# Optimization experiments

Measured on AMD Instinct MI355X. Metric: run time of the kernel, lower is better.

The kernel has to match this reference:

```python
import jax, jax.numpy as jnp
import numpy as np

B, S, D = 16, 1024, 1024
LR = 0.01  # manual SGD step size inside TTT


def setup_inputs() -> dict:
    key = jax.random.key(0)
    ks = jax.random.split(key, 9)
    s = 1.0 / np.sqrt(D)  # nn.Linear default init range
    lin = lambda k: jax.random.uniform(k, (D, D), jnp.float32, -s, s)
    return {
        "x": jax.random.normal(ks[0], (B, S, D), jnp.float32),
        "noise": jax.random.normal(ks[1], (B, S, D), jnp.float32),
        "alpha1": jax.random.normal(ks[2], (D,), jnp.float32),
        "alpha2": jax.random.normal(ks[3], (D,), jnp.float32),
        "W_map": lin(ks[4]),    # TTT.mapping weight (updated online)
        "W_state": lin(ks[5]),  # TTT.State weight
        "W_probe": lin(ks[6]),  # TTT.Probe weight
        "W_p1": lin(ks[7]),     # GatingUnit.proj_1
        "W_p2": lin(ks[8]),     # GatingUnit.proj_2
    }


def reference(x, noise, alpha1, alpha2, W_map, W_state, W_probe, W_p1, W_p2):
    # --- TTT: sequential per-timestep test-time training, expressed as a scan ---
    def ttt(h):
        xs = jnp.swapaxes(h, 0, 1)       # [S, B, D]
        ns = jnp.swapaxes(noise, 0, 1)   # [S, B, D]

        def step(W, inp):
            x_t, n_t = inp                       # [B, D]
            state = x_t @ W_state.T              # State(x_t)
            tv = state + n_t                     # train_view = state + randn
            err = tv @ W.T - state               # mapping(train_view) - label_view
            # d(mse)/dW for y = x W^T, loss = mean(err^2) over B*D elements
            grad = (2.0 / (x_t.shape[0] * x_t.shape[1])) * (err.T @ tv)
            Wn = W - LR * grad                   # manual SGD update
            readout = (x_t @ W_probe.T) @ Wn.T   # mapping(Probe(x_t)) with updated W
            return Wn, readout

        _, outs = jax.lax.scan(step, W_map, (xs, ns))
        return jnp.swapaxes(outs, 0, 1)          # [B, S, D]

    # --- TensorMapperBlock ---
    res = x
    h = jnp.tanh(alpha1 * x)          # VecDyT norm_1
    x1 = ttt(h) + res
    res2 = x1
    h2 = jnp.tanh(alpha2 * x1)        # VecDyT norm_2
    u = jax.nn.gelu(h2 @ W_p1.T, approximate=False)  # torch nn.GELU (exact)
    v = h2 @ W_p2.T
    return u * v + res2
```

## Files before the change

kernel.cpp:

```cpp
#include <hip/hip_runtime.h>
#include <math.h>


typedef __bf16 bf16;
typedef __attribute__((ext_vector_type(8))) __bf16 bf16x8;
typedef __attribute__((ext_vector_type(4))) __bf16 bf16x4;
typedef __attribute__((ext_vector_type(4))) float f32x4;

#define LAM 1.220703125e-6f

enum { M_TV = 0, M_P = 1, M_E0 = 2, M_CT = 3, M_KP = 4, M_OUT = 5, M_U = 6 };

struct GA {
  const bf16* A;  int lda;
  const bf16* B;  int ldb;
  const bf16* A2; int lda2;
  const bf16* B2; int ldb2;
  int K;
  const float* noise;
  const float* xin;
  const float* alpha2;
  const bf16* TVb;
  const bf16* Vb;
  bf16* H2b;
  float* outf;
  bf16* Cb; int ldc;
};

#define GLOAD_LDS16(gp, lp)                                                   \
  __builtin_amdgcn_global_load_lds(                                           \
      (const __attribute__((address_space(1))) unsigned int*)(gp),            \
      (__attribute__((address_space(3))) unsigned int*)(lp), 16, 0, 0)

__device__ __forceinline__ void stage_tiles(const bf16* __restrict__ Ap, int lda,
                                            const bf16* __restrict__ Bp, int ldb,
                                            int k0, bf16* As, bf16* Bs, int tid) {
  const int wv = tid >> 6, lane = tid & 63;
#pragma unroll
  for (int i = 0; i < 2; ++i) {
    int idx = (wv << 6) + lane + (i << 8);
    int row = idx >> 2;
    int k8 = (idx & 3) << 3;
    int lbase = ((wv << 6) + (i << 8)) << 3;
    GLOAD_LDS16(Ap + (size_t)row * lda + k0 + k8, As + lbase);
    GLOAD_LDS16(Bp + (size_t)row * ldb + k0 + k8, Bs + lbase);
  }
}

__device__ __forceinline__ void compute_step(const bf16* As, const bf16* Bs,
                                             int wr, int wc, int m, int ko,
                                             f32x4 acc[4][4]) {
  bf16x8 af[4], bfr[4];
#pragma unroll
  for (int i = 0; i < 4; ++i)
    af[i] = *(const bf16x8*)(As + (wr + i * 16 + m) * 32 + ko * 8);
#pragma unroll
  for (int j = 0; j < 4; ++j)
    bfr[j] = *(const bf16x8*)(Bs + (wc + j * 16 + m) * 32 + ko * 8);
#pragma unroll
  for (int i = 0; i < 4; ++i) {
#pragma unroll
    for (int j = 0; j < 4; ++j)
      acc[i][j] =
          __builtin_amdgcn_mfma_f32_16x16x32_bf16(af[i], bfr[j], acc[i][j], 0, 0, 0);
  }
}

template <int MODE>
__device__ __forceinline__ void stage_sel(const GA& g, int s, int steps1,
                                          const bf16* A1, const bf16* B1,
                                          const bf16* A2, const bf16* B2,
                                          bf16* Asb, bf16* Bsb, int tid) {
  if constexpr (MODE == M_OUT) {
    if (s >= steps1) {
      stage_tiles(A2, g.lda2, B2, g.ldb2, (s - steps1) << 5, Asb, Bsb, tid);
      return;
    }
  }
  stage_tiles(A1, g.lda, B1, g.ldb, s << 5, Asb, Bsb, tid);
}

template <int MODE>
__global__ __launch_bounds__(256) void gemm_nt(GA g) {
  __shared__ __attribute__((aligned(16))) bf16 As0[128 * 32];
  __shared__ __attribute__((aligned(16))) bf16 Bs0[128 * 32];
  __shared__ __attribute__((aligned(16))) bf16 As1[128 * 32];
  __shared__ __attribute__((aligned(16))) bf16 Bs1[128 * 32];

  const int bx = blockIdx.x, by = blockIdx.y, bz = blockIdx.z;
  const int c0 = bx << 7;
  const int r0 = by << 7;
  if constexpr (MODE == M_KP) {
    if (c0 > r0) return;
  }

  size_t zA = 0, zB = 0, zC = 0;
  if constexpr (MODE == M_CT) { zA = (size_t)bz << 10; zB = zA; zC = (size_t)bz << 20; }
  if constexpr (MODE == M_KP) { zA = (size_t)bz << 20; zB = zA; zC = zA; }
  if constexpr (MODE == M_OUT) { zA = (size_t)bz << 20; zB = (size_t)bz << 10; }

  const int tid = threadIdx.x;
  const int lane = tid & 63, wv = tid >> 6;
  const int wr = (wv >> 1) << 6, wc = (wv & 1) << 6;
  const int m = lane & 15, ko = lane >> 4;

  f32x4 acc[4][4];
#pragma unroll
  for (int i = 0; i < 4; ++i) {
#pragma unroll
    for (int j = 0; j < 4; ++j) acc[i][j] = (f32x4){0.f, 0.f, 0.f, 0.f};
  }

  int K1 = g.K;
  if constexpr (MODE == M_OUT) K1 = r0 + 128;
  const int steps1 = K1 >> 5;

  const bf16* A1 = g.A + zA + (size_t)r0 * g.lda;
  const bf16* B1 = g.B + zB + (size_t)c0 * g.ldb;
  const bf16* A2 = nullptr;
  const bf16* B2 = nullptr;
  int total = steps1;
  if constexpr (MODE == M_OUT) {
    A2 = g.A2 + zA + (size_t)r0 * g.lda2;
    B2 = g.B2 + zA + (size_t)c0 * g.ldb2;
    total += 32;
  }

  stage_sel<MODE>(g, 0, steps1, A1, B1, A2, B2, As0, Bs0, tid);
  __syncthreads();

  int s = 0;
  for (; s + 2 < total; s += 2) {
    stage_sel<MODE>(g, s + 1, steps1, A1, B1, A2, B2, As1, Bs1, tid);
    compute_step(As0, Bs0, wr, wc, m, ko, acc);
    __syncthreads();
    stage_sel<MODE>(g, s + 2, steps1, A1, B1, A2, B2, As0, Bs0, tid);
    compute_step(As1, Bs1, wr, wc, m, ko, acc);
    __syncthreads();
  }
  if (s + 1 < total) {
    stage_sel<MODE>(g, s + 1, steps1, A1, B1, A2, B2, As1, Bs1, tid);
    compute_step(As0, Bs0, wr, wc, m, ko, acc);
    __syncthreads();
    compute_step(As1, Bs1, wr, wc, m, ko, acc);
  } else {
    compute_step(As0, Bs0, wr, wc, m, ko, acc);
  }

#pragma unroll
  for (int i = 0; i < 4; ++i) {
#pragma unroll
    for (int j = 0; j < 4; ++j) {
      const int gc = c0 + wc + j * 16 + m;
#pragma unroll
      for (int rg = 0; rg < 4; ++rg) {
        const int grl = r0 + wr + i * 16 + ko * 4 + rg;
        float v = acc[i][j][rg];
        if constexpr (MODE == M_TV) {
          int t = grl >> 4, b = grl & 15;
          float tv = v + g.noise[((size_t)b << 20) + ((size_t)t << 10) + gc];
          g.Cb[(size_t)grl * g.ldc + gc] = (bf16)tv;
        } else if constexpr (MODE == M_P) {
          g.Cb[(size_t)grl * g.ldc + gc] = (bf16)v;
        } else if constexpr (MODE == M_CT) {
          g.Cb[zC + (size_t)grl * g.ldc + gc] = (bf16)v;
        } else if constexpr (MODE == M_E0) {
          int t = grl >> 4, b = grl & 15;
          size_t ni = ((size_t)b << 20) + ((size_t)t << 10) + gc;
          float tvv = (float)g.TVb[(size_t)grl * 1024 + gc];
          float e0 = v - (tvv - g.noise[ni]);
          g.Cb[(size_t)grl * g.ldc + gc] = (bf16)e0;
        } else if constexpr (MODE == M_KP) {
          float sv = ((gc >> 4) <= (grl >> 4)) ? (-LAM * v) : 0.0f;
          g.Cb[zC + (size_t)grl * g.ldc + gc] = (bf16)sv;
        } else if constexpr (MODE == M_OUT) {
          int rgl = (bz << 10) + grl;
          int t = rgl >> 4, b = rgl & 15;
          size_t oi = ((size_t)b << 20) + ((size_t)t << 10) + gc;
          float x1 = v + g.xin[oi];
          g.outf[oi] = x1;
          g.H2b[oi] = (bf16)tanhf(g.alpha2[gc] * x1);
        } else if constexpr (MODE == M_U) {
          size_t oi = (size_t)grl * 1024 + gc;
          float u = v;
          float gl = 0.5f * u * (1.0f + erff(u * 0.70710678118654752f));
          g.outf[oi] = gl * (float)g.Vb[oi] + g.outf[oi];
        }
      }
    }
  }
}

__global__ void ew_convert(const float* w0, const float* w1, const float* w2,
                           const float* w3, const float* w4, bf16* dst) {
  int gid = blockIdx.x * 256 + threadIdx.x;
  int i4 = gid << 2;
  int mm = i4 >> 20;
  const float* src = (mm == 0) ? w0 : (mm == 1) ? w1 : (mm == 2) ? w2
                     : (mm == 3) ? w3 : w4;
  int off = i4 & 1048575;
  float4 v = *(const float4*)(src + off);
  bf16x4 o;
  o[0] = (bf16)v.x; o[1] = (bf16)v.y; o[2] = (bf16)v.z; o[3] = (bf16)v.w;
  *(bf16x4*)(dst + i4) = o;
}

__global__ void ew_h1(const float* __restrict__ x, const float* __restrict__ a1,
                      bf16* __restrict__ H) {
  int gid = blockIdx.x * 256 + threadIdx.x;
  int i4 = gid << 2;
  int d = i4 & 1023;
  int t = (i4 >> 10) & 1023;
  int b = i4 >> 20;
  float4 xv = *(const float4*)(x + i4);
  float4 av = *(const float4*)(a1 + d);
  bf16x4 o;
  o[0] = (bf16)tanhf(av.x * xv.x);
  o[1] = (bf16)tanhf(av.y * xv.y);
  o[2] = (bf16)tanhf(av.z * xv.z);
  o[3] = (bf16)tanhf(av.w * xv.w);
  *(bf16x4*)(H + (((size_t)((t << 4) + b)) << 10) + d) = o;
}

__global__ void prefix_s(const bf16* __restrict__ C, bf16* __restrict__ S,
                         const bf16* __restrict__ W0) {
  int gid = blockIdx.x * 256 + threadIdx.x;
  size_t base = (size_t)gid << 2;
  bf16x4 wv = *(const bf16x4*)(W0 + base);
  float w0 = (float)wv[0], w1 = (float)wv[1], w2 = (float)wv[2],
        w3 = (float)wv[3];
  float ac0 = 0.f, ac1 = 0.f, ac2 = 0.f, ac3 = 0.f;
#pragma unroll
  for (int j = 0; j < 16; ++j) {
    size_t off = ((size_t)j << 20) + base;
    bf16x4 c = *(const bf16x4*)(C + off);
    bf16x4 o;
    o[0] = (bf16)(w0 - LAM * ac0);
    o[1] = (bf16)(w1 - LAM * ac1);
    o[2] = (bf16)(w2 - LAM * ac2);
    o[3] = (bf16)(w3 - LAM * ac3);
    *(bf16x4*)(S + off) = o;
    ac0 += (float)c[0]; ac1 += (float)c[1];
    ac2 += (float)c[2]; ac3 += (float)c[3];
  }
}

__global__ __launch_bounds__(256) void tr_e0(const bf16* __restrict__ in,
                                             bf16* __restrict__ out) {
  __shared__ bf16 tile[64][72];
  int c0 = blockIdx.x << 6;
  int r0 = blockIdx.y << 6;
  int tid = threadIdx.x;
  int lr = tid >> 4;
  int lc = (tid & 15) << 2;
#pragma unroll
  for (int ph = 0; ph < 4; ++ph) {
    int row = lr + (ph << 4);
    bf16x4 v = *(const bf16x4*)(in + (size_t)(r0 + row) * 1024 + c0 + lc);
    *(bf16x4*)(&tile[row][lc]) = v;
  }
  __syncthreads();
#pragma unroll
  for (int ph = 0; ph < 4; ++ph) {
    int oc = lr + (ph << 4);
    bf16x4 v;
    v[0] = tile[lc + 0][oc];
    v[1] = tile[lc + 1][oc];
    v[2] = tile[lc + 2][oc];
    v[3] = tile[lc + 3][oc];
    *(bf16x4*)(out + (size_t)(c0 + oc) * 16384 + r0 + lc) = v;
  }
}

extern "C" void kernel_launch(void* const* d_in, const int* in_sizes, int n_in,
                              void* d_out, int out_size, void* d_ws,
                              size_t ws_size, hipStream_t stream) {
  (void)in_sizes; (void)n_in; (void)out_size;
  const float* x = (const float*)d_in[0];
  const float* noise = (const float*)d_in[1];
  const float* a1 = (const float*)d_in[2];
  const float* a2 = (const float*)d_in[3];
  const float* Wmap = (const float*)d_in[4];
  const float* Wst = (const float*)d_in[5];
  const float* Wpr = (const float*)d_in[6];
  const float* Wp1 = (const float*)d_in[7];
  const float* Wp2 = (const float*)d_in[8];
  float* out = (float*)d_out;

  const size_t MB32 = (size_t)16384 * 1024 * 2;
  const size_t NEED = 5 * MB32 + 5 * (size_t)1048576 * 2;
  if (ws_size < NEED) return;

  char* ws = (char*)d_ws;
  bf16* s0 = (bf16*)(ws);
  bf16* s1 = (bf16*)(ws + MB32);
  bf16* s2 = (bf16*)(ws + 2 * MB32);
  bf16* s3 = (bf16*)(ws + 3 * MB32);
  bf16* s4 = (bf16*)(ws + 4 * MB32);
  bf16* Wcat = (bf16*)(ws + 5 * MB32);
  bf16* Wb0 = Wcat;
  bf16* Wsb = Wcat + (1 << 20);
  bf16* Wpb = Wcat + 2 * (1 << 20);
  bf16* W1b = Wcat + 3 * (1 << 20);
  bf16* W2b = Wcat + 4 * (1 << 20);

  ew_convert<<<5120, 256, 0, stream>>>(Wmap, Wst, Wpr, Wp1, Wp2, Wcat);
  ew_h1<<<16384, 256, 0, stream>>>(x, a1, s0);

  {
    GA g{};
    g.A = s0; g.lda = 1024; g.B = Wsb; g.ldb = 1024; g.K = 1024;
    g.noise = noise; g.Cb = s1; g.ldc = 1024;
    gemm_nt<M_TV><<<dim3(8, 128), 256, 0, stream>>>(g);
  }
  {
    GA g{};
    g.A = s0; g.lda = 1024; g.B = Wpb; g.ldb = 1024; g.K = 1024;
    g.Cb = s2; g.ldc = 1024;
    gemm_nt<M_P><<<dim3(8, 128), 256, 0, stream>>>(g);
  }
  {
    GA g{};
    g.A = s1; g.lda = 1024; g.B = Wb0; g.ldb = 1024; g.K = 1024;
    g.noise = noise; g.TVb = s1; g.Cb = s0; g.ldc = 1024;
    gemm_nt<M_E0><<<dim3(8, 128), 256, 0, stream>>>(g);
  }
  tr_e0<<<dim3(16, 256), 256, 0, stream>>>(s0, s3);
  tr_e0<<<dim3(16, 256), 256, 0, stream>>>(s1, s4);

  {
    GA g{};
    g.A = s3; g.lda = 16384; g.B = s4; g.ldb = 16384; g.K = 1024;
    g.Cb = s0; g.ldc = 1024;
    gemm_nt<M_CT><<<dim3(8, 8, 16), 256, 0, stream>>>(g);
  }
  prefix_s<<<1024, 256, 0, stream>>>(s0, s0, Wb0);

  {
    GA g{};
    g.A = s2; g.lda = 1024; g.B = s1; g.ldb = 1024; g.K = 1024;
    g.Cb = s4; g.ldc = 1024;
    gemm_nt<M_KP><<<dim3(8, 8, 16), 256, 0, stream>>>(g);
  }
  {
    GA g{};
    g.A = s4; g.lda = 1024;
    g.B = s3; g.ldb = 16384;
    g.A2 = s2; g.lda2 = 1024;
    g.B2 = s0; g.ldb2 = 1024;
    g.xin = x; g.outf = out;
    g.alpha2 = a2; g.H2b = s1;
    gemm_nt<M_OUT><<<dim3(8, 8, 16), 256, 0, stream>>>(g);
  }

  {
    GA g{};
    g.A = s1; g.lda = 1024; g.B = W2b; g.ldb = 1024; g.K = 1024;
    g.Cb = s0; g.ldc = 1024;
    gemm_nt<M_P><<<dim3(8, 128), 256, 0, stream>>>(g);
  }
  {
    GA g{};
    g.A = s1; g.lda = 1024; g.B = W1b; g.ldb = 1024; g.K = 1024;
    g.Vb = s0; g.outf = out;
    gemm_nt<M_U><<<dim3(8, 128), 256, 0, stream>>>(g);
  }
}
```

Measured before the change: 892.7 us.

## Deepen GEMM pipeline to 4 LDS buffers with vmcnt waits, swizzle, and tile remap

After: 853.0 us. 4.5% less time.

```diff
diff --git a/kernel.cpp b/kernel.cpp
--- a/kernel.cpp
+++ b/kernel.cpp
@@ -32,31 +32,37 @@
       (const __attribute__((address_space(1))) unsigned int*)(gp),            \
       (__attribute__((address_space(3))) unsigned int*)(lp), 16, 0, 0)
 
+#define WAIT_BARRIER(N)                                                       \
+  do {                                                                        \
+    asm volatile("s_waitcnt vmcnt(" #N ")\n\ts_barrier" ::: "memory");        \
+    __builtin_amdgcn_sched_barrier(0);                                        \
+  } while (0)
+
 __device__ __forceinline__ void stage_tiles(const bf16* __restrict__ Ap, int lda,
                                             const bf16* __restrict__ Bp, int ldb,
                                             int k0, bf16* As, bf16* Bs, int tid) {
-  const int wv = tid >> 6, lane = tid & 63;
-#pragma unroll
-  for (int i = 0; i < 2; ++i) {
-    int idx = (wv << 6) + lane + (i << 8);
-    int row = idx >> 2;
-    int k8 = (idx & 3) << 3;
-    int lbase = ((wv << 6) + (i << 8)) << 3;
-    GLOAD_LDS16(Ap + (size_t)row * lda + k0 + k8, As + lbase);
-    GLOAD_LDS16(Bp + (size_t)row * ldb + k0 + k8, Bs + lbase);
+#pragma unroll
+  for (int rr = 0; rr < 2; ++rr) {
+    int c = tid + (rr << 8);
+    int row = c >> 2;
+    int kb = (c & 3) ^ ((c >> 3) & 3);
+    int lbase = ((tid & 192) + (rr << 8)) << 3;
+    GLOAD_LDS16(Ap + (size_t)row * lda + k0 + (kb << 3), As + lbase);
+    GLOAD_LDS16(Bp + (size_t)row * ldb + k0 + (kb << 3), Bs + lbase);
   }
 }
 
 __device__ __forceinline__ void compute_step(const bf16* As, const bf16* Bs,
-                                             int wr, int wc, int m, int ko,
+                                             int wr, int wc, int m, int gsw,
                                              f32x4 acc[4][4]) {
   bf16x8 af[4], bfr[4];
 #pragma unroll
   for (int i = 0; i < 4; ++i)
-    af[i] = *(const bf16x8*)(As + (wr + i * 16 + m) * 32 + ko * 8);
+    af[i] = *(const bf16x8*)(As + (wr + i * 16 + m) * 32 + (gsw << 3));
 #pragma unroll
   for (int j = 0; j < 4; ++j)
-    bfr[j] = *(const bf16x8*)(Bs + (wc + j * 16 + m) * 32 + ko * 8);
+    bfr[j] = *(const bf16x8*)(Bs + (wc + j * 16 + m) * 32 + (gsw << 3));
+  __builtin_amdgcn_s_setprio(1);
 #pragma unroll
   for (int i = 0; i < 4; ++i) {
 #pragma unroll
@@ -64,6 +70,7 @@
       acc[i][j] =
           __builtin_amdgcn_mfma_f32_16x16x32_bf16(af[i], bfr[j], acc[i][j], 0, 0, 0);
   }
+  __builtin_amdgcn_s_setprio(0);
 }
 
 template <int MODE>
@@ -82,12 +89,18 @@
 
 template <int MODE>
 __global__ __launch_bounds__(256) void gemm_nt(GA g) {
-  __shared__ __attribute__((aligned(16))) bf16 As0[128 * 32];
-  __shared__ __attribute__((aligned(16))) bf16 Bs0[128 * 32];
-  __shared__ __attribute__((aligned(16))) bf16 As1[128 * 32];
-  __shared__ __attribute__((aligned(16))) bf16 Bs1[128 * 32];
-
-  const int bx = blockIdx.x, by = blockIdx.y, bz = blockIdx.z;
+  __shared__ __attribute__((aligned(16))) bf16 As[4][128 * 32];
+  __shared__ __attribute__((aligned(16))) bf16 Bs[4][128 * 32];
+
+  const int gx = gridDim.x, gy = gridDim.y;
+  const int nwg = gx * gy * (int)gridDim.z;
+  int flat = blockIdx.x + gx * (blockIdx.y + gy * blockIdx.z);
+  int swz = (flat & 7) * (nwg >> 3) + (flat >> 3);
+  const int bx = swz % gx;
+  int t1v = swz / gx;
+  const int by = t1v % gy;
+  const int bz = t1v / gy;
+
   const int c0 = bx << 7;
   const int r0 = by << 7;
   if constexpr (MODE == M_KP) {
@@ -103,6 +116,7 @@
   const int lane = tid & 63, wv = tid >> 6;
   const int wr = (wv >> 1) << 6, wc = (wv & 1) << 6;
   const int m = lane & 15, ko = lane >> 4;
+  const int gsw = ko ^ ((m >> 1) & 3);
 
   f32x4 acc[4][4];
 #pragma unroll
@@ -126,26 +140,21 @@
     total += 32;
   }
 
-  stage_sel<MODE>(g, 0, steps1, A1, B1, A2, B2, As0, Bs0, tid);
-  __syncthreads();
+  stage_sel<MODE>(g, 0, steps1, A1, B1, A2, B2, As[0], Bs[0], tid);
+  stage_sel<MODE>(g, 1, steps1, A1, B1, A2, B2, As[1], Bs[1], tid);
 
   int s = 0;
-  for (; s + 2 < total; s += 2) {
-    stage_sel<MODE>(g, s + 1, steps1, A1, B1, A2, B2, As1, Bs1, tid);
-    compute_step(As0, Bs0, wr, wc, m, ko, acc);
-    __syncthreads();
-    stage_sel<MODE>(g, s + 2, steps1, A1, B1, A2, B2, As0, Bs0, tid);
-    compute_step(As1, Bs1, wr, wc, m, ko, acc);
-    __syncthreads();
-  }
-  if (s + 1 < total) {
-    stage_sel<MODE>(g, s + 1, steps1, A1, B1, A2, B2, As1, Bs1, tid);
-    compute_step(As0, Bs0, wr, wc, m, ko, acc);
-    __syncthreads();
-    compute_step(As1, Bs1, wr, wc, m, ko, acc);
-  } else {
-    compute_step(As0, Bs0, wr, wc, m, ko, acc);
-  }
+  for (; s < total - 2; ++s) {
+    const int rn = (s + 2) & 3;
+    stage_sel<MODE>(g, s + 2, steps1, A1, B1, A2, B2, As[rn], Bs[rn], tid);
+    WAIT_BARRIER(8);
+    compute_step(As[s & 3], Bs[s & 3], wr, wc, m, gsw, acc);
+  }
+  WAIT_BARRIER(4);
+  compute_step(As[s & 3], Bs[s & 3], wr, wc, m, gsw, acc);
+  ++s;
+  WAIT_BARRIER(0);
+  compute_step(As[s & 3], Bs[s & 3], wr, wc, m, gsw, acc);
 
 #pragma unroll
   for (int i = 0; i < 4; ++i) {
```
